# Optimization experiments

Measured on AMD Instinct MI355X. Metric: run time of the kernel, lower is better.

## Reference

```python
import jax, jax.numpy as jnp
import numpy as np

N = 100000      # nodes
E = 1600000     # edges (avg degree 16)
D = 128         # feature dim (in_dim == out_dim)
ALPHA = 0.1     # initial-residual mixing
BETA = 0.5      # identity-mapping / linear mixing


def setup_inputs() -> dict:
    key = jax.random.key(0)
    k1, k2, k3, k4, k5 = jax.random.split(key, 5)
    features = jax.random.normal(k1, (N, D), dtype=jnp.float32)
    initial_features = jax.random.normal(k2, (N, D), dtype=jnp.float32)
    # xavier_uniform with relu gain sqrt(2): bound = gain * sqrt(6/(fan_in+fan_out))
    bound = np.sqrt(2.0) * np.sqrt(6.0 / (D + D))
    W = jax.random.uniform(k5, (D, D), dtype=jnp.float32, minval=-bound, maxval=bound)
    src = jax.random.randint(k3, (E,), 0, N, dtype=jnp.int32)
    dst = jax.random.randint(k4, (E,), 0, N, dtype=jnp.int32)
    return {"features": features, "initial_features": initial_features,
            "W": W, "src": src, "dst": dst}


def reference(features, initial_features, W, src, dst):
    # symmetric degree normalization (edge weights are all ones)
    degs = jax.ops.segment_sum(jnp.ones((E,), features.dtype), dst, num_segments=N)
    norm = jnp.power(jnp.maximum(degs, 1.0), -0.5)[:, None]          # [N,1]
    h = features * norm                                               # [N,D]
    # message passing: m_e = h[src_e] * w_e (w=1); aggregate sum into dst
    agg = jax.ops.segment_sum(h[src], dst, num_segments=N)            # [N,D]
    h = agg * norm
    # alpha initial-residual, beta identity-mapped linear combine
    h = (1.0 - ALPHA) * h + ALPHA * initial_features
    h = (1.0 - BETA) * h + BETA * (h @ W.T)
    return jax.nn.relu(h)
```

## Files before the change

kernel.cpp:

```cpp
#include <hip/hip_runtime.h>
#include <math.h>

#define D 128
#define THREADS 256
#define BS 512
#define MAXB 1024
#define CAP 9216
#define BIN_T 512
#define EPT 16
#define BIN_CHUNK (BIN_T * EPT)

typedef __attribute__((ext_vector_type(8))) short s16x8;
typedef __attribute__((ext_vector_type(4))) float f32x4;
typedef __attribute__((ext_vector_type(4))) float f4;
typedef __attribute__((ext_vector_type(4))) unsigned u4;

__device__ __forceinline__ unsigned short f2bf(float f) {
    unsigned u = __float_as_uint(f);
    u += 0x7FFFu + ((u >> 16) & 1u);
    return (unsigned short)(u >> 16);
}
__device__ __forceinline__ float bflo(unsigned u) { return __uint_as_float(u << 16); }
__device__ __forceinline__ float bfhi(unsigned u) { return __uint_as_float(u & 0xFFFF0000u); }

__global__ __launch_bounds__(THREADS) void k_init(int* __restrict__ bcur,
                                                  int* __restrict__ ocnt, int nbuck) {
    const int b = blockIdx.x * THREADS + threadIdx.x;
    if (b < nbuck) bcur[b] = b * CAP;
    if (b == 0) *ocnt = 0;
}

__global__ __launch_bounds__(BIN_T) void k_bin(const int* __restrict__ src,
                                               const int* __restrict__ dst,
                                               int* __restrict__ bcur,
                                               unsigned* __restrict__ ebuf,
                                               int2* __restrict__ ovf,
                                               int* __restrict__ ocnt,
                                               int E, int nbuck) {
    __shared__ int lh[MAXB];
    __shared__ int lbase[MAXB];
    const int tid = threadIdx.x;
    for (int b = tid; b < nbuck; b += BIN_T) lh[b] = 0;
    __syncthreads();
    const int base = blockIdx.x * BIN_CHUNK;
    int bk[EPT];
    unsigned pk[EPT];
#pragma unroll
    for (int k = 0; k < EPT; ++k) {
        const int e = base + k * BIN_T + tid;
        if (e < E) {
            const int d = dst[e];
            bk[k] = d >> 9;
            pk[k] = ((unsigned)src[e] << 9) | (unsigned)(d & (BS - 1));
            atomicAdd(&lh[bk[k]], 1);
        } else {
            bk[k] = -1;
        }
    }
    __syncthreads();
    for (int b = tid; b < nbuck; b += BIN_T) {
        const int v = lh[b];
        lbase[b] = v ? atomicAdd(&bcur[b], v) : 0;
        lh[b] = 0;
    }
    __syncthreads();
#pragma unroll
    for (int k = 0; k < EPT; ++k) {
        if (bk[k] >= 0) {
            const int pos = lbase[bk[k]] + atomicAdd(&lh[bk[k]], 1);
            if (pos < (bk[k] + 1) * CAP) {
                ebuf[pos] = pk[k];
            } else {
                const int op = atomicAdd(ocnt, 1);
                ovf[op] = make_int2((int)pk[k], bk[k]);
            }
        }
    }
}

__global__ __launch_bounds__(BS) void k_csr(const unsigned* __restrict__ ebuf,
                                            const int* __restrict__ bcur,
                                            const int2* __restrict__ ovf,
                                            const int* __restrict__ ocnt,
                                            const float* __restrict__ features,
                                            int* __restrict__ csr,
                                            int2* __restrict__ offdeg,
                                            float* __restrict__ normf,
                                            uint4* __restrict__ hb,
                                            int n, int nbuck) {
    __shared__ int cnt[BS];
    __shared__ int ex[BS];
    const int b = blockIdx.x, tid = threadIdx.x;
    const int lo = b * CAP;
    const int hi = min(bcur[b], lo + CAP);
    const int oc = *ocnt;
    cnt[tid] = 0;
    __syncthreads();
    for (int e = lo + tid; e < hi; e += BS)
        atomicAdd(&cnt[ebuf[e] & (BS - 1)], 1);
    for (int i = tid; i < oc; i += BS) {
        const int2 o = ovf[i];
        if (o.y == b) atomicAdd(&cnt[(unsigned)o.x & (BS - 1)], 1);
    }
    __syncthreads();
    const int deg = cnt[tid];
    ex[tid] = deg;
    __syncthreads();
    for (int s = 1; s < BS; s <<= 1) {
        const int t = (tid >= s) ? ex[tid - s] : 0;
        __syncthreads();
        ex[tid] += t;
        __syncthreads();
    }
    const int excl = ex[tid] - deg;
    const int node = b * BS + tid;
    const float nrm = rsqrtf(fmaxf((float)deg, 1.0f));
    if (node < n) {
        offdeg[node] = make_int2(lo + excl, deg);
        normf[node] = nrm;
    }
    cnt[tid] = excl;
    __syncthreads();
    ex[tid] = __float_as_int(nrm);
    const int csrEnd = nbuck * CAP;
    for (int e = lo + tid; e < hi; e += BS) {
        const unsigned pe = ebuf[e];
        const int p = atomicAdd(&cnt[pe & (BS - 1)], 1);
        if (lo + p < csrEnd) csr[lo + p] = (int)(pe >> 9);
    }
    for (int i = tid; i < oc; i += BS) {
        const int2 o = ovf[i];
        if (o.y == b) {
            const unsigned pe = (unsigned)o.x;
            const int p = atomicAdd(&cnt[pe & (BS - 1)], 1);
            if (lo + p < csrEnd) csr[lo + p] = (int)(pe >> 9);
        }
    }
    __syncthreads();
    const f4* fp = (const f4*)features;
    for (int idx = tid; idx < BS * 16; idx += BS) {
        const int nl = idx >> 4;
        const int gnode = b * BS + nl;
        if (gnode >= n) break;
        const float nv = __int_as_float(ex[nl]);
        const size_t C = (size_t)gnode * 16 + (idx & 15);
        const f4 a = __builtin_nontemporal_load(fp + C * 2);
        const f4 bb = __builtin_nontemporal_load(fp + C * 2 + 1);
        uint4 o;
        o.x = f2bf(a.x * nv) | ((unsigned)f2bf(a.y * nv) << 16);
        o.y = f2bf(a.z * nv) | ((unsigned)f2bf(a.w * nv) << 16);
        o.z = f2bf(bb.x * nv) | ((unsigned)f2bf(bb.y * nv) << 16);
        o.w = f2bf(bb.z * nv) | ((unsigned)f2bf(bb.w * nv) << 16);
        hb[C] = o;
    }
}

__global__ __launch_bounds__(THREADS) void k_gather_csr(
    const uint4* __restrict__ hb, const float* __restrict__ initf,
    const int2* __restrict__ offdeg, const int* __restrict__ csr,
    const float* __restrict__ normf, uint4* __restrict__ tb, int n) {
    const int g = (blockIdx.x * THREADS + threadIdx.x) >> 4;
    if (g >= n) return;
    const int gl = threadIdx.x & 15;

    float acc[8] = {0.f, 0.f, 0.f, 0.f, 0.f, 0.f, 0.f, 0.f};

#define ROW(S)                                                      \
    {                                                               \
        const uint4 r = hb[(size_t)(S)*16 + gl];                    \
        acc[0] += bflo(r.x); acc[1] += bfhi(r.x);                   \
        acc[2] += bflo(r.y); acc[3] += bfhi(r.y);                   \
        acc[4] += bflo(r.z); acc[5] += bfhi(r.z);                   \
        acc[6] += bflo(r.w); acc[7] += bfhi(r.w);                   \
    }
    const int2 od = offdeg[g];
    const int begin = od.x, end = od.x + od.y;
    int j = begin;
    for (; j + 4 <= end; j += 4) {
        const int s0 = csr[j], s1 = csr[j + 1], s2 = csr[j + 2], s3 = csr[j + 3];
        ROW(s0); ROW(s1); ROW(s2); ROW(s3);
    }
    for (; j < end; ++j) ROW(csr[j]);
#undef ROW

    const float nv = 0.9f * normf[g];
    const f4* iv = (const f4*)(initf + (size_t)g * D);
    const f4 i0 = __builtin_nontemporal_load(iv + gl * 2);
    const f4 i1 = __builtin_nontemporal_load(iv + gl * 2 + 1);
    float t[8];
    t[0] = nv * acc[0] + 0.1f * i0.x; t[1] = nv * acc[1] + 0.1f * i0.y;
    t[2] = nv * acc[2] + 0.1f * i0.z; t[3] = nv * acc[3] + 0.1f * i0.w;
    t[4] = nv * acc[4] + 0.1f * i1.x; t[5] = nv * acc[5] + 0.1f * i1.y;
    t[6] = nv * acc[6] + 0.1f * i1.z; t[7] = nv * acc[7] + 0.1f * i1.w;
    u4 o;
    o.x = f2bf(t[0]) | ((unsigned)f2bf(t[1]) << 16);
    o.y = f2bf(t[2]) | ((unsigned)f2bf(t[3]) << 16);
    o.z = f2bf(t[4]) | ((unsigned)f2bf(t[5]) << 16);
    o.w = f2bf(t[6]) | ((unsigned)f2bf(t[7]) << 16);
    __builtin_nontemporal_store(o, (u4*)tb + (size_t)g * 16 + gl);
}

__device__ __forceinline__ void stage_M(const float* __restrict__ W,
                                        uint4* __restrict__ sMt, int tid) {
    for (int c = tid; c < D * 16; c += THREADS) {
        const int j = c >> 4, kc = c & 15;
        const float* wr = W + j * D + kc * 8;
        float m[8];
#pragma unroll
        for (int q = 0; q < 8; ++q) m[q] = 0.5f * wr[q];
        const int dj = j - kc * 8;
        if (dj >= 0 && dj < 8) m[dj] += 0.5f;
        uint4 o;
        o.x = f2bf(m[0]) | ((unsigned)f2bf(m[1]) << 16);
        o.y = f2bf(m[2]) | ((unsigned)f2bf(m[3]) << 16);
        o.z = f2bf(m[4]) | ((unsigned)f2bf(m[5]) << 16);
        o.w = f2bf(m[6]) | ((unsigned)f2bf(m[7]) << 16);
        sMt[j * 16 + (kc ^ (j & 7))] = o;
    }
}

__device__ __forceinline__ void gemm_tile(const uint4* __restrict__ sMt,
                                          const uint4* __restrict__ sT,
                                          float* __restrict__ out,
                                          int base, int n, int lane, int wave) {
    const int l15 = lane & 15, lq = lane >> 4;
    const int mt = wave & 1, ntb = (wave >> 1) * 4;
    const int nr = mt * 16 + l15;
    s16x8 a[4];
#pragma unroll
    for (int ks = 0; ks < 4; ++ks)
        a[ks] = *reinterpret_cast<const s16x8*>(
            &sT[nr * 16 + ((ks * 4 + lq) ^ (nr & 7))]);

#pragma unroll
    for (int tnt = 0; tnt < 4; ++tnt) {
        const int nt = ntb + tnt;
        const int jr = nt * 16 + l15;
        f32x4 c = {0.f, 0.f, 0.f, 0.f};
#pragma unroll
        for (int ks = 0; ks < 4; ++ks) {
            const s16x8 b = *reinterpret_cast<const s16x8*>(
                &sMt[jr * 16 + ((ks * 4 + lq) ^ (jr & 7))]);
            c = __builtin_amdgcn_mfma_f32_16x16x32_bf16(a[ks], b, c, 0, 0, 0);
        }
        const int col = nt * 16 + l15;
        const int row0 = base + mt * 16 + lq * 4;
#pragma unroll
        for (int r = 0; r < 4; ++r) {
            const int node = row0 + r;
            if (node < n)
                __builtin_nontemporal_store(fmaxf(c[r], 0.f),
                                            &out[(size_t)node * D + col]);
        }
    }
}

__global__ __launch_bounds__(THREADS) void k_gemm_tb(
    const float* __restrict__ W, const uint4* __restrict__ tb,
    float* __restrict__ out, int n, int numTiles) {
    __shared__ uint4 sMt[D * 16];
    __shared__ uint4 sT[32 * 16];
    const int tid = threadIdx.x;
    stage_M(W, sMt, tid);
    __syncthreads();

    const int sn = tid >> 3;
    const int c0 = (tid & 7) * 2;
    const int wave = tid >> 6, lane = tid & 63;

    for (int tile = blockIdx.x; tile < numTiles; tile += gridDim.x) {
        const int base = tile << 5;
        {
            const int node = base + sn;
#pragma unroll
            for (int s = 0; s < 2; ++s) {
                const int cc = c0 + s;
                uint4 o;
                if (node < n) {
                    const u4 t = __builtin_nontemporal_load(
                        (const u4*)tb + (size_t)node * 16 + cc);
                    o.x = t.x; o.y = t.y; o.z = t.z; o.w = t.w;
                } else {
                    o.x = o.y = o.z = o.w = 0u;
                }
                sT[sn * 16 + (cc ^ (sn & 7))] = o;
            }
        }
        __syncthreads();
        gemm_tile(sMt, sT, out, base, n, lane, wave);
        __syncthreads();
    }
}

__global__ __launch_bounds__(THREADS) void k_build1(
    const int* __restrict__ src, const int* __restrict__ dst,
    int* __restrict__ head, int2* __restrict__ p, int E) {
    int e = blockIdx.x * THREADS + threadIdx.x;
    if (e < E) {
        int nx = atomicExch(&head[dst[e]], e);
        p[e] = make_int2(nx, src[e]);
    }
}

__global__ __launch_bounds__(THREADS) void k_normwalk1(
    const int* __restrict__ head, const int2* __restrict__ p,
    float* __restrict__ normf, int n) {
    int i = blockIdx.x * THREADS + threadIdx.x;
    if (i >= n) return;
    int c = head[i], cnt = 0;
    while (c >= 0) { ++cnt; c = p[c].x; }
    normf[i] = rsqrtf(fmaxf((float)cnt, 1.0f));
}

__global__ __launch_bounds__(THREADS) void k_gatherchain(
    const float* __restrict__ features, const float* __restrict__ initf,
    const int* __restrict__ head, const int2* __restrict__ p,
    const float* __restrict__ normf, float* __restrict__ out, int n) {
    const int g = (blockIdx.x * THREADS + threadIdx.x) >> 4;
    if (g >= n) return;
    const int gl = threadIdx.x & 15;
    float acc[8] = {0.f, 0.f, 0.f, 0.f, 0.f, 0.f, 0.f, 0.f};
    int c = head[g];
    while (c >= 0) {
        const int2 pc = p[c];
        const float w = normf[pc.y];
        const float4* fr = (const float4*)(features + (size_t)pc.y * D);
        const float4 f0 = fr[gl * 2], f1 = fr[gl * 2 + 1];
        acc[0] += f0.x * w; acc[1] += f0.y * w;
        acc[2] += f0.z * w; acc[3] += f0.w * w;
        acc[4] += f1.x * w; acc[5] += f1.y * w;
        acc[6] += f1.z * w; acc[7] += f1.w * w;
        c = pc.x;
    }
    const float nv = 0.9f * normf[g];
    const float4* iv = (const float4*)(initf + (size_t)g * D);
    const float4 i0 = iv[gl * 2], i1 = iv[gl * 2 + 1];
    float4 t0, t1;
    t0.x = nv * acc[0] + 0.1f * i0.x; t0.y = nv * acc[1] + 0.1f * i0.y;
    t0.z = nv * acc[2] + 0.1f * i0.z; t0.w = nv * acc[3] + 0.1f * i0.w;
    t1.x = nv * acc[4] + 0.1f * i1.x; t1.y = nv * acc[5] + 0.1f * i1.y;
    t1.z = nv * acc[6] + 0.1f * i1.z; t1.w = nv * acc[7] + 0.1f * i1.w;
    float4* orow = (float4*)(out + (size_t)g * D);
    orow[gl * 2] = t0;
    orow[gl * 2 + 1] = t1;
}

__global__ __launch_bounds__(THREADS) void k_gemm_ip(
    const float* __restrict__ W, float* __restrict__ out, int n, int numTiles) {
    __shared__ uint4 sMt[D * 16];
    __shared__ uint4 sT[32 * 16];
    const int tid = threadIdx.x;
    stage_M(W, sMt, tid);
    __syncthreads();
    const int sn = tid >> 3;
    const int c0 = (tid & 7) * 2;
    const int wave = tid >> 6, lane = tid & 63;
    for (int tile = blockIdx.x; tile < numTiles; tile += gridDim.x) {
        const int base = tile << 5;
        {
            const int node = base + sn;
#pragma unroll
            for (int s = 0; s < 2; ++s) {
                const int cc = c0 + s;
                uint4 o;
                if (node < n) {
                    const float4* tr = (const float4*)(out + (size_t)node * D);
                    const float4 a = tr[cc * 2], b = tr[cc * 2 + 1];
                    o.x = f2bf(a.x) | ((unsigned)f2bf(a.y) << 16);
                    o.y = f2bf(a.z) | ((unsigned)f2bf(a.w) << 16);
                    o.z = f2bf(b.x) | ((unsigned)f2bf(b.y) << 16);
                    o.w = f2bf(b.z) | ((unsigned)f2bf(b.w) << 16);
                } else {
                    o.x = o.y = o.z = o.w = 0u;
                }
                sT[sn * 16 + (cc ^ (sn & 7))] = o;
            }
        }
        __syncthreads();
        gemm_tile(sMt, sT, out, base, n, lane, wave);
        __syncthreads();
    }
}

extern "C" void kernel_launch(void* const* d_in, const int* in_sizes, int n_in,
                              void* d_out, int out_size, void* d_ws, size_t ws_size,
                              hipStream_t stream) {
    const float* features = (const float*)d_in[0];
    const float* initf    = (const float*)d_in[1];
    const float* W        = (const float*)d_in[2];
    const int*   src      = (const int*)d_in[3];
    const int*   dst      = (const int*)d_in[4];
    float* out = (float*)d_out;

    const int n = in_sizes[0] / D;
    const int E = in_sizes[3];
    if (n <= 0) return;

    const int nbuck = (n + BS - 1) / BS;
    const int numTiles = (n + 31) >> 5;
    const int gridT = numTiles < 1024 ? numTiles : 1024;
    const int gridG = (int)(((size_t)n * 16 + THREADS - 1) / THREADS);

    const size_t odA  = ((size_t)n * 8 + 15) & ~(size_t)15;
    const size_t nA   = ((size_t)n * 4 + 15) & ~(size_t)15;
    const size_t bA   = ((size_t)MAXB * 4 + 16);
    const size_t slabA = ((size_t)nbuck * CAP * 4 + 15) & ~(size_t)15;
    const size_t hbA  = (size_t)n * 256;
    const size_t tbA  = (size_t)n * 256;
    const size_t needMain = odA + nA + bA + 2 * slabA + hbA + tbA;

    if (nbuck <= MAXB && n <= (1 << 23) && ws_size >= needMain) {
        char* w = (char*)d_ws;
        int2*     offdeg = (int2*)w;              w += odA;
        float*    normf  = (float*)w;             w += nA;
        int*      bcur   = (int*)w;
        int*      ocnt   = (int*)(w + (size_t)MAXB * 4);  w += bA;
        unsigned* ebuf   = (unsigned*)w;          w += slabA;
        int*      csr    = (int*)w;               w += slabA;
        uint4*    hb     = (uint4*)w;             w += hbA;
        uint4*    tb     = (uint4*)w;
        int2*     ovf    = (int2*)tb;

        k_init<<<(nbuck + THREADS - 1) / THREADS, THREADS, 0, stream>>>(bcur, ocnt, nbuck);
        k_bin<<<(E + BIN_CHUNK - 1) / BIN_CHUNK, BIN_T, 0, stream>>>(
            src, dst, bcur, ebuf, ovf, ocnt, E, nbuck);
        k_csr<<<nbuck, BS, 0, stream>>>(ebuf, bcur, ovf, ocnt, features,
                                        csr, offdeg, normf, hb, n, nbuck);
        k_gather_csr<<<gridG, THREADS, 0, stream>>>(hb, initf, offdeg, csr, normf, tb, n);
        k_gemm_tb<<<gridT, THREADS, 0, stream>>>(W, tb, out, n, numTiles);
    } else {
        const size_t pA = ((size_t)E * 8 + 15) & ~(size_t)15;
        float* normf = (float*)d_ws;
        int*   head  = (int*)((char*)d_ws + nA);
        int2*  p     = (int2*)((char*)d_ws + 2 * nA);
        if (ws_size < 2 * nA + pA) return;
        hipMemsetAsync(head, 0xFF, (size_t)n * 4, stream);
        k_build1<<<(E + THREADS - 1) / THREADS, THREADS, 0, stream>>>(src, dst, head, p, E);
        k_normwalk1<<<(n + THREADS - 1) / THREADS, THREADS, 0, stream>>>(head, p, normf, n);
        k_gatherchain<<<gridG, THREADS, 0, stream>>>(features, initf, head, p, normf, out, n);
        k_gemm_ip<<<gridT, THREADS, 0, stream>>>(W, out, n, numTiles);
    }
}
```

Measured before the change: 168.6 us.

## Split feature scaling into own kernel, vectorize binning and CSR index loads

Binning now processes 4 contiguous edges per thread with vector loads and uses two sub-histogram slots per bucket to reduce shared atomic contention. The CSR build caches bucket edges in shared memory to avoid re-reading global memory. Feature normalization and bf16 conversion move into a separate fully parallel kernel instead of running inside the 196-block CSR kernel. Gather loads neighbor indices as int4, which may be misaligned since segment offsets are arbitrary.

```diff
diff --git a/kernel.cpp b/kernel.cpp
--- a/kernel.cpp
+++ b/kernel.cpp
@@ -7,7 +7,7 @@
 #define MAXB 1024
 #define CAP 9216
 #define BIN_T 512
-#define EPT 16
+#define EPT 4
 #define BIN_CHUNK (BIN_T * EPT)
 
 typedef __attribute__((ext_vector_type(8))) short s16x8;
@@ -37,37 +37,56 @@
                                                int2* __restrict__ ovf,
                                                int* __restrict__ ocnt,
                                                int E, int nbuck) {
-    __shared__ int lh[MAXB];
-    __shared__ int lbase[MAXB];
+    __shared__ int lh[2 * MAXB];
+    __shared__ int lbase[2 * MAXB];
     const int tid = threadIdx.x;
-    for (int b = tid; b < nbuck; b += BIN_T) lh[b] = 0;
-    __syncthreads();
-    const int base = blockIdx.x * BIN_CHUNK;
+    const int sub = tid & 1;
+    for (int b = tid; b < 2 * nbuck; b += BIN_T) lh[b] = 0;
+    __syncthreads();
+    const int e0 = blockIdx.x * BIN_CHUNK + tid * EPT;
     int bk[EPT];
     unsigned pk[EPT];
-#pragma unroll
-    for (int k = 0; k < EPT; ++k) {
-        const int e = base + k * BIN_T + tid;
-        if (e < E) {
-            const int d = dst[e];
-            bk[k] = d >> 9;
-            pk[k] = ((unsigned)src[e] << 9) | (unsigned)(d & (BS - 1));
-            atomicAdd(&lh[bk[k]], 1);
-        } else {
-            bk[k] = -1;
+    if (e0 + EPT <= E) {
+        const int4 d4 = *reinterpret_cast<const int4*>(dst + e0);
+        const int4 s4 = *reinterpret_cast<const int4*>(src + e0);
+        const int dd[4] = {d4.x, d4.y, d4.z, d4.w};
+        const int ss[4] = {s4.x, s4.y, s4.z, s4.w};
+#pragma unroll
+        for (int k = 0; k < EPT; ++k) {
+            bk[k] = dd[k] >> 9;
+            pk[k] = ((unsigned)ss[k] << 9) | (unsigned)(dd[k] & (BS - 1));
+            atomicAdd(&lh[bk[k] * 2 + sub], 1);
+        }
+    } else {
+#pragma unroll
+        for (int k = 0; k < EPT; ++k) {
+            const int e = e0 + k;
+            if (e < E) {
+                const int d = dst[e];
+                bk[k] = d >> 9;
+                pk[k] = ((unsigned)src[e] << 9) | (unsigned)(d & (BS - 1));
+                atomicAdd(&lh[bk[k] * 2 + sub], 1);
+            } else {
+                bk[k] = -1;
+            }
         }
     }
     __syncthreads();
     for (int b = tid; b < nbuck; b += BIN_T) {
-        const int v = lh[b];
-        lbase[b] = v ? atomicAdd(&bcur[b], v) : 0;
-        lh[b] = 0;
+        const int c0 = lh[b * 2], c1 = lh[b * 2 + 1];
+        const int v = c0 + c1;
+        const int base = v ? atomicAdd(&bcur[b], v) : 0;
+        lbase[b * 2] = base;
+        lbase[b * 2 + 1] = base + c0;
+        lh[b * 2] = 0;
+        lh[b * 2 + 1] = 0;
     }
     __syncthreads();
 #pragma unroll
     for (int k = 0; k < EPT; ++k) {
         if (bk[k] >= 0) {
-            const int pos = lbase[bk[k]] + atomicAdd(&lh[bk[k]], 1);
+            const int slot = bk[k] * 2 + sub;
+            const int pos = lbase[slot] + atomicAdd(&lh[slot], 1);
             if (pos < (bk[k] + 1) * CAP) {
                 ebuf[pos] = pk[k];
             } else {
@@ -82,22 +101,24 @@
                                             const int* __restrict__ bcur,
                                             const int2* __restrict__ ovf,
                                             const int* __restrict__ ocnt,
-                                            const float* __restrict__ features,
                                             int* __restrict__ csr,
                                             int2* __restrict__ offdeg,
                                             float* __restrict__ normf,
-                                            uint4* __restrict__ hb,
                                             int n, int nbuck) {
+    __shared__ unsigned sedge[CAP];
     __shared__ int cnt[BS];
     __shared__ int ex[BS];
     const int b = blockIdx.x, tid = threadIdx.x;
     const int lo = b * CAP;
-    const int hi = min(bcur[b], lo + CAP);
+    const int m = min(bcur[b], lo + CAP) - lo;
     const int oc = *ocnt;
     cnt[tid] = 0;
     __syncthreads();
-    for (int e = lo + tid; e < hi; e += BS)
-        atomicAdd(&cnt[ebuf[e] & (BS - 1)], 1);
+    for (int i = tid; i < m; i += BS) {
+        const unsigned pe = ebuf[lo + i];
+        sedge[i] = pe;
+        atomicAdd(&cnt[pe & (BS - 1)], 1);
+    }
     for (int i = tid; i < oc; i += BS) {
         const int2 o = ovf[i];
         if (o.y == b) atomicAdd(&cnt[(unsigned)o.x & (BS - 1)], 1);
@@ -114,17 +135,15 @@
     }
     const int excl = ex[tid] - deg;
     const int node = b * BS + tid;
-    const float nrm = rsqrtf(fmaxf((float)deg, 1.0f));
     if (node < n) {
         offdeg[node] = make_int2(lo + excl, deg);
-        normf[node] = nrm;
+        normf[node] = rsqrtf(fmaxf((float)deg, 1.0f));
     }
     cnt[tid] = excl;
     __syncthreads();
-    ex[tid] = __float_as_int(nrm);
     const int csrEnd = nbuck * CAP;
-    for (int e = lo + tid; e < hi; e += BS) {
-        const unsigned pe = ebuf[e];
+    for (int i = tid; i < m; i += BS) {
+        const unsigned pe = sedge[i];
         const int p = atomicAdd(&cnt[pe & (BS - 1)], 1);
         if (lo + p < csrEnd) csr[lo + p] = (int)(pe >> 9);
     }
@@ -136,23 +155,23 @@
             if (lo + p < csrEnd) csr[lo + p] = (int)(pe >> 9);
         }
     }
-    __syncthreads();
-    const f4* fp = (const f4*)features;
-    for (int idx = tid; idx < BS * 16; idx += BS) {
-        const int nl = idx >> 4;
-        const int gnode = b * BS + nl;
-        if (gnode >= n) break;
-        const float nv = __int_as_float(ex[nl]);
-        const size_t C = (size_t)gnode * 16 + (idx & 15);
-        const f4 a = __builtin_nontemporal_load(fp + C * 2);
-        const f4 bb = __builtin_nontemporal_load(fp + C * 2 + 1);
-        uint4 o;
-        o.x = f2bf(a.x * nv) | ((unsigned)f2bf(a.y * nv) << 16);
-        o.y = f2bf(a.z * nv) | ((unsigned)f2bf(a.w * nv) << 16);
-        o.z = f2bf(bb.x * nv) | ((unsigned)f2bf(bb.y * nv) << 16);
-        o.w = f2bf(bb.z * nv) | ((unsigned)f2bf(bb.w * nv) << 16);
-        hb[C] = o;
-    }
+}
+
+__global__ __launch_bounds__(THREADS) void k_scale(
+    const float* __restrict__ f, const float* __restrict__ nrm,
+    uint4* __restrict__ hb, int n) {
+    int c = blockIdx.x * THREADS + threadIdx.x;
+    if (c >= n * 16) return;
+    float nv = nrm[c >> 4];
+    const f4* fp = (const f4*)f;
+    const f4 a = __builtin_nontemporal_load(fp + c * 2);
+    const f4 b = __builtin_nontemporal_load(fp + c * 2 + 1);
+    uint4 o;
+    o.x = f2bf(a.x * nv) | ((unsigned)f2bf(a.y * nv) << 16);
+    o.y = f2bf(a.z * nv) | ((unsigned)f2bf(a.w * nv) << 16);
+    o.z = f2bf(b.x * nv) | ((unsigned)f2bf(b.y * nv) << 16);
+    o.w = f2bf(b.z * nv) | ((unsigned)f2bf(b.w * nv) << 16);
+    hb[c] = o;
 }
 
 __global__ __launch_bounds__(THREADS) void k_gather_csr(
@@ -176,9 +195,15 @@
     const int2 od = offdeg[g];
     const int begin = od.x, end = od.x + od.y;
     int j = begin;
+    for (; j + 8 <= end; j += 8) {
+        const int4 a4 = *reinterpret_cast<const int4*>(csr + j);
+        const int4 b4 = *reinterpret_cast<const int4*>(csr + j + 4);
+        ROW(a4.x); ROW(a4.y); ROW(a4.z); ROW(a4.w);
+        ROW(b4.x); ROW(b4.y); ROW(b4.z); ROW(b4.w);
+    }
     for (; j + 4 <= end; j += 4) {
-        const int s0 = csr[j], s1 = csr[j + 1], s2 = csr[j + 2], s3 = csr[j + 3];
-        ROW(s0); ROW(s1); ROW(s2); ROW(s3);
+        const int4 a4 = *reinterpret_cast<const int4*>(csr + j);
+        ROW(a4.x); ROW(a4.y); ROW(a4.z); ROW(a4.w);
     }
     for (; j < end; ++j) ROW(csr[j]);
 #undef ROW
@@ -424,8 +449,9 @@
         k_init<<<(nbuck + THREADS - 1) / THREADS, THREADS, 0, stream>>>(bcur, ocnt, nbuck);
         k_bin<<<(E + BIN_CHUNK - 1) / BIN_CHUNK, BIN_T, 0, stream>>>(
             src, dst, bcur, ebuf, ovf, ocnt, E, nbuck);
-        k_csr<<<nbuck, BS, 0, stream>>>(ebuf, bcur, ovf, ocnt, features,
-                                        csr, offdeg, normf, hb, n, nbuck);
+        k_csr<<<nbuck, BS, 0, stream>>>(ebuf, bcur, ovf, ocnt, csr, offdeg, normf, n, nbuck);
+        k_scale<<<(n * 16 + THREADS - 1) / THREADS, THREADS, 0, stream>>>(
+            features, normf, hb, n);
         k_gather_csr<<<gridG, THREADS, 0, stream>>>(hb, initf, offdeg, csr, normf, tb, n);
         k_gemm_tb<<<gridT, THREADS, 0, stream>>>(W, tb, out, n, numTiles);
     } else {
```

New measurement: 173.0 us. 1.03x slower.

## Use per-block bucket subslabs, stage edges in LDS, and build CSR in place

Applied to the files above, without the earlier changes.

Edge binning now runs in 128 blocks. Each block counts its chunk, then writes into a private per-(bucket, block) sub-slab, so the global per-bucket atomic cursors and the init kernel go away. The CSR kernel prefix-sums the per-block counts, copies the bucket's edges into a large LDS buffer, and scatters source indices back into the same slab. This removes the separate CSR buffer and the second global read of the edge list. The gather kernel also loads neighbour indices as int4 vectors, 8 at a time. Costs: only 128 binning blocks, each reading dst twice; about 57KB of LDS per CSR block, which limits occupancy; and int4 loads from CSR offsets that are not 16-byte aligned.

```diff
diff --git a/kernel.cpp b/kernel.cpp
--- a/kernel.cpp
+++ b/kernel.cpp
@@ -5,10 +5,8 @@
 #define THREADS 256
 #define BS 512
 #define MAXB 1024
-#define CAP 9216
-#define BIN_T 512
-#define EPT 16
-#define BIN_CHUNK (BIN_T * EPT)
+#define NBLK 128
+#define SMAX 14336
 
 typedef __attribute__((ext_vector_type(8))) short s16x8;
 typedef __attribute__((ext_vector_type(4))) float f32x4;
@@ -23,81 +21,82 @@
 __device__ __forceinline__ float bflo(unsigned u) { return __uint_as_float(u << 16); }
 __device__ __forceinline__ float bfhi(unsigned u) { return __uint_as_float(u & 0xFFFF0000u); }
 
-__global__ __launch_bounds__(THREADS) void k_init(int* __restrict__ bcur,
-                                                  int* __restrict__ ocnt, int nbuck) {
-    const int b = blockIdx.x * THREADS + threadIdx.x;
-    if (b < nbuck) bcur[b] = b * CAP;
-    if (b == 0) *ocnt = 0;
-}
-
-__global__ __launch_bounds__(BIN_T) void k_bin(const int* __restrict__ src,
-                                               const int* __restrict__ dst,
-                                               int* __restrict__ bcur,
-                                               unsigned* __restrict__ ebuf,
-                                               int2* __restrict__ ovf,
-                                               int* __restrict__ ocnt,
-                                               int E, int nbuck) {
+__global__ __launch_bounds__(BS) void k_bin(const int* __restrict__ src,
+                                            const int* __restrict__ dst,
+                                            unsigned* __restrict__ slab,
+                                            int* __restrict__ bcnt2,
+                                            int2* __restrict__ ovf,
+                                            int* __restrict__ ocnt,
+                                            int E, int nbuck,
+                                            int chunk, int subcap, int capt) {
     __shared__ int lh[MAXB];
-    __shared__ int lbase[MAXB];
-    const int tid = threadIdx.x;
-    for (int b = tid; b < nbuck; b += BIN_T) lh[b] = 0;
-    __syncthreads();
-    const int base = blockIdx.x * BIN_CHUNK;
-    int bk[EPT];
-    unsigned pk[EPT];
-#pragma unroll
-    for (int k = 0; k < EPT; ++k) {
-        const int e = base + k * BIN_T + tid;
-        if (e < E) {
-            const int d = dst[e];
-            bk[k] = d >> 9;
-            pk[k] = ((unsigned)src[e] << 9) | (unsigned)(d & (BS - 1));
-            atomicAdd(&lh[bk[k]], 1);
+    const int blk = blockIdx.x, tid = threadIdx.x;
+    for (int b = tid; b < nbuck; b += BS) lh[b] = 0;
+    __syncthreads();
+    const int e0 = blk * chunk;
+    const int e1 = min(e0 + chunk, E);
+    for (int e = e0 + tid; e < e1; e += BS)
+        atomicAdd(&lh[dst[e] >> 9], 1);
+    __syncthreads();
+    for (int b = tid; b < nbuck; b += BS) {
+        bcnt2[b * NBLK + blk] = min(lh[b], subcap);
+        lh[b] = 0;
+    }
+    __syncthreads();
+    for (int e = e0 + tid; e < e1; e += BS) {
+        const int d = dst[e];
+        const int b = d >> 9;
+        const unsigned pk = ((unsigned)src[e] << 9) | (unsigned)(d & (BS - 1));
+        const int p = atomicAdd(&lh[b], 1);
+        if (p < subcap) {
+            slab[(size_t)b * capt + blk * subcap + p] = pk;
         } else {
-            bk[k] = -1;
-        }
-    }
-    __syncthreads();
-    for (int b = tid; b < nbuck; b += BIN_T) {
-        const int v = lh[b];
-        lbase[b] = v ? atomicAdd(&bcur[b], v) : 0;
-        lh[b] = 0;
-    }
-    __syncthreads();
-#pragma unroll
-    for (int k = 0; k < EPT; ++k) {
-        if (bk[k] >= 0) {
-            const int pos = lbase[bk[k]] + atomicAdd(&lh[bk[k]], 1);
-            if (pos < (bk[k] + 1) * CAP) {
-                ebuf[pos] = pk[k];
-            } else {
-                const int op = atomicAdd(ocnt, 1);
-                ovf[op] = make_int2((int)pk[k], bk[k]);
-            }
-        }
-    }
-}
-
-__global__ __launch_bounds__(BS) void k_csr(const unsigned* __restrict__ ebuf,
-                                            const int* __restrict__ bcur,
+            const int op = atomicAdd(ocnt, 1);
+            ovf[op] = make_int2((int)pk, b);
+        }
+    }
+}
+
+__global__ __launch_bounds__(BS) void k_csr(unsigned* __restrict__ slab,
+                                            const int* __restrict__ bcnt2,
                                             const int2* __restrict__ ovf,
                                             const int* __restrict__ ocnt,
                                             const float* __restrict__ features,
-                                            int* __restrict__ csr,
                                             int2* __restrict__ offdeg,
                                             float* __restrict__ normf,
                                             uint4* __restrict__ hb,
-                                            int n, int nbuck) {
+                                            int n, int nbuck, int subcap, int capt) {
+    __shared__ unsigned sedge[SMAX];
+    __shared__ int sbase[NBLK + 1];
     __shared__ int cnt[BS];
     __shared__ int ex[BS];
     const int b = blockIdx.x, tid = threadIdx.x;
-    const int lo = b * CAP;
-    const int hi = min(bcur[b], lo + CAP);
+    const size_t lo = (size_t)b * capt;
+
+    if (tid < NBLK) sbase[tid + 1] = bcnt2[b * NBLK + tid];
+    if (tid == 0) sbase[0] = 0;
+    __syncthreads();
+    for (int s = 1; s < NBLK; s <<= 1) {
+        int v = 0;
+        if (tid < NBLK && tid >= s) v = sbase[tid + 1 - s];
+        __syncthreads();
+        if (tid < NBLK) sbase[tid + 1] += v;
+        __syncthreads();
+    }
+    const int m = sbase[NBLK];
+    {
+        const int w = tid >> 6, l = tid & 63;
+        for (int i = w; i < NBLK; i += BS / 64) {
+            const int s0 = sbase[i], L = sbase[i + 1] - s0;
+            for (int j = l; j < L; j += 64)
+                sedge[s0 + j] = slab[lo + (size_t)i * subcap + j];
+        }
+    }
+    cnt[tid] = 0;
+    __syncthreads();
+    for (int i = tid; i < m; i += BS)
+        atomicAdd(&cnt[sedge[i] & (BS - 1)], 1);
     const int oc = *ocnt;
-    cnt[tid] = 0;
-    __syncthreads();
-    for (int e = lo + tid; e < hi; e += BS)
-        atomicAdd(&cnt[ebuf[e] & (BS - 1)], 1);
     for (int i = tid; i < oc; i += BS) {
         const int2 o = ovf[i];
         if (o.y == b) atomicAdd(&cnt[(unsigned)o.x & (BS - 1)], 1);
@@ -116,24 +115,26 @@
     const int node = b * BS + tid;
     const float nrm = rsqrtf(fmaxf((float)deg, 1.0f));
     if (node < n) {
-        offdeg[node] = make_int2(lo + excl, deg);
+        offdeg[node] = make_int2((int)lo + excl, deg);
         normf[node] = nrm;
     }
     cnt[tid] = excl;
     __syncthreads();
     ex[tid] = __float_as_int(nrm);
-    const int csrEnd = nbuck * CAP;
-    for (int e = lo + tid; e < hi; e += BS) {
-        const unsigned pe = ebuf[e];
+    const size_t slabEnd = (size_t)nbuck * capt;
+    for (int i = tid; i < m; i += BS) {
+        const unsigned pe = sedge[i];
         const int p = atomicAdd(&cnt[pe & (BS - 1)], 1);
-        if (lo + p < csrEnd) csr[lo + p] = (int)(pe >> 9);
+        const size_t q = lo + p;
+        if (q < slabEnd) slab[q] = pe >> 9;
     }
     for (int i = tid; i < oc; i += BS) {
         const int2 o = ovf[i];
         if (o.y == b) {
             const unsigned pe = (unsigned)o.x;
             const int p = atomicAdd(&cnt[pe & (BS - 1)], 1);
-            if (lo + p < csrEnd) csr[lo + p] = (int)(pe >> 9);
+            const size_t q = lo + p;
+            if (q < slabEnd) slab[q] = pe >> 9;
         }
     }
     __syncthreads();
@@ -176,9 +177,15 @@
     const int2 od = offdeg[g];
     const int begin = od.x, end = od.x + od.y;
     int j = begin;
+    for (; j + 8 <= end; j += 8) {
+        const int4 a4 = *reinterpret_cast<const int4*>(csr + j);
+        const int4 b4 = *reinterpret_cast<const int4*>(csr + j + 4);
+        ROW(a4.x); ROW(a4.y); ROW(a4.z); ROW(a4.w);
+        ROW(b4.x); ROW(b4.y); ROW(b4.z); ROW(b4.w);
+    }
     for (; j + 4 <= end; j += 4) {
-        const int s0 = csr[j], s1 = csr[j + 1], s2 = csr[j + 2], s3 = csr[j + 3];
-        ROW(s0); ROW(s1); ROW(s2); ROW(s3);
+        const int4 a4 = *reinterpret_cast<const int4*>(csr + j);
+        ROW(a4.x); ROW(a4.y); ROW(a4.z); ROW(a4.w);
     }
     for (; j < end; ++j) ROW(csr[j]);
 #undef ROW
@@ -401,32 +408,37 @@
     const int gridT = numTiles < 1024 ? numTiles : 1024;
     const int gridG = (int)(((size_t)n * 16 + THREADS - 1) / THREADS);
 
+    const int chunk = (E + NBLK - 1) / NBLK;
+    const float mu = (float)chunk / (float)nbuck;
+    const int subcap = (int)(mu + 5.0f * sqrtf(mu)) + 8;
+    const int capt = NBLK * subcap;
+
     const size_t odA  = ((size_t)n * 8 + 15) & ~(size_t)15;
     const size_t nA   = ((size_t)n * 4 + 15) & ~(size_t)15;
-    const size_t bA   = ((size_t)MAXB * 4 + 16);
-    const size_t slabA = ((size_t)nbuck * CAP * 4 + 15) & ~(size_t)15;
+    const size_t b2A  = ((size_t)nbuck * NBLK * 4 + 15) & ~(size_t)15;
+    const size_t slabA = ((size_t)nbuck * capt * 4 + 15) & ~(size_t)15;
     const size_t hbA  = (size_t)n * 256;
     const size_t tbA  = (size_t)n * 256;
-    const size_t needMain = odA + nA + bA + 2 * slabA + hbA + tbA;
-
-    if (nbuck <= MAXB && n <= (1 << 23) && ws_size >= needMain) {
+    const size_t needMain = odA + nA + b2A + 16 + slabA + hbA + tbA;
+
+    if (nbuck <= MAXB && n <= (1 << 23) && capt <= SMAX && ws_size >= needMain) {
         char* w = (char*)d_ws;
         int2*     offdeg = (int2*)w;              w += odA;
         float*    normf  = (float*)w;             w += nA;
-        int*      bcur   = (int*)w;
-        int*      ocnt   = (int*)(w + (size_t)MAXB * 4);  w += bA;
-        unsigned* ebuf   = (unsigned*)w;          w += slabA;
-        int*      csr    = (int*)w;               w += slabA;
+        int*      bcnt2  = (int*)w;               w += b2A;
+        int*      ocnt   = (int*)w;               w += 16;
+        unsigned* slab   = (unsigned*)w;          w += slabA;
         uint4*    hb     = (uint4*)w;             w += hbA;
         uint4*    tb     = (uint4*)w;
         int2*     ovf    = (int2*)tb;
 
-        k_init<<<(nbuck + THREADS - 1) / THREADS, THREADS, 0, stream>>>(bcur, ocnt, nbuck);
-        k_bin<<<(E + BIN_CHUNK - 1) / BIN_CHUNK, BIN_T, 0, stream>>>(
-            src, dst, bcur, ebuf, ovf, ocnt, E, nbuck);
-        k_csr<<<nbuck, BS, 0, stream>>>(ebuf, bcur, ovf, ocnt, features,
-                                        csr, offdeg, normf, hb, n, nbuck);
-        k_gather_csr<<<gridG, THREADS, 0, stream>>>(hb, initf, offdeg, csr, normf, tb, n);
+        hipMemsetAsync(ocnt, 0, 4, stream);
+        k_bin<<<NBLK, BS, 0, stream>>>(src, dst, slab, bcnt2, ovf, ocnt,
+                                       E, nbuck, chunk, subcap, capt);
+        k_csr<<<nbuck, BS, 0, stream>>>(slab, bcnt2, ovf, ocnt, features,
+                                        offdeg, normf, hb, n, nbuck, subcap, capt);
+        k_gather_csr<<<gridG, THREADS, 0, stream>>>(hb, initf, offdeg,
+                                                    (const int*)slab, normf, tb, n);
         k_gemm_tb<<<gridT, THREADS, 0, stream>>>(W, tb, out, n, numTiles);
     } else {
         const size_t pA = ((size_t)E * 8 + 15) & ~(size_t)15;
```

Result: slower. 178.0 us (+5.6%).
